# Kernel tuning notes

Hardware: AMD Instinct MI355X
Metric: run time of the kernel (lower is better)

Reference implementation:

```python
import jax, jax.numpy as jnp
import numpy as np

N_NODES = 50000
N_EDGES = 800000
NODE_IN = 10
EDGE_IN = 7
H = 128
N_LAYERS = 6
OUT_DIM = 3


def setup_inputs() -> dict:
    key = jax.random.key(0)
    ks = jax.random.split(key, 32)
    s = 0.05
    inp = {
        "x": jax.random.normal(ks[0], (N_NODES, NODE_IN), jnp.float32),
        "edge_attr": jax.random.normal(ks[1], (N_EDGES, EDGE_IN), jnp.float32),
        "edge_index": jax.random.randint(ks[2], (2, N_EDGES), 0, N_NODES, jnp.int32),
        "bc_disp": jax.random.uniform(ks[3], (N_NODES, 1), jnp.float32),
        "bc_rot": jax.random.uniform(ks[4], (N_NODES, 1), jnp.float32),
        # node encoder: MLP(10, [H], H)
        "ne_w1": jax.random.normal(ks[5], (NODE_IN, H), jnp.float32) * s,
        "ne_b1": jnp.zeros((H,), jnp.float32),
        "ne_w2": jax.random.normal(ks[6], (H, H), jnp.float32) * s,
        "ne_b2": jnp.zeros((H,), jnp.float32),
        # edge encoder: MLP(7, [H], H)
        "ee_w1": jax.random.normal(ks[7], (EDGE_IN, H), jnp.float32) * s,
        "ee_b1": jnp.zeros((H,), jnp.float32),
        "ee_w2": jax.random.normal(ks[8], (H, H), jnp.float32) * s,
        "ee_b2": jnp.zeros((H,), jnp.float32),
        # 6 GraphNetworkLayers: edge model (3H -> H), node model (2H -> H)
        "mp_ew": jax.random.normal(ks[9], (N_LAYERS, 3 * H, H), jnp.float32) * s,
        "mp_eb": jnp.zeros((N_LAYERS, H), jnp.float32),
        "mp_nw": jax.random.normal(ks[10], (N_LAYERS, 2 * H, H), jnp.float32) * s,
        "mp_nb": jnp.zeros((N_LAYERS, H), jnp.float32),
        "d_w1": jax.random.normal(ks[11], (H, H), jnp.float32) * s,
        "d_b1": jnp.zeros((H,), jnp.float32),
        "d_w2": jax.random.normal(ks[12], (H, 64), jnp.float32) * s,
        "d_b2": jnp.zeros((64,), jnp.float32),
        "d_w3": jax.random.normal(ks[13], (64, OUT_DIM), jnp.float32) * (s * 5.0),
        "d_b3": jnp.full((OUT_DIM,), 0.5, jnp.float32),
    }
    return inp


def reference(x, edge_attr, edge_index, bc_disp, bc_rot,
              ne_w1, ne_b1, ne_w2, ne_b2,
              ee_w1, ee_b1, ee_w2, ee_b2,
              mp_ew, mp_eb, mp_nw, mp_nb,
              d_w1, d_b1, d_w2, d_b2, d_w3, d_b3):
    # encode nodes and edges (Linear -> ReLU -> Linear)
    h = jax.nn.relu(x @ ne_w1 + ne_b1) @ ne_w2 + ne_b2            # [N, H]
    e = jax.nn.relu(edge_attr @ ee_w1 + ee_b1) @ ee_w2 + ee_b2    # [E, H]
    src = edge_index[0]
    dst = edge_index[1]
    # 6 residual message-passing layers: gather -> edge MLP -> scatter-add -> node MLP
    for l in range(N_LAYERS):
        msg_in = jnp.concatenate([h[src], h[dst], e], axis=-1)    # [E, 3H]
        msg = jax.nn.relu(msg_in @ mp_ew[l] + mp_eb[l])           # [E, H]
        agg = jax.ops.segment_sum(msg, dst, num_segments=N_NODES)  # [N, H] (aggr='add')
        upd = jax.nn.relu(jnp.concatenate([h, agg], axis=-1) @ mp_nw[l] + mp_nb[l])
        h = h + upd                                               # residual
    # decode: Linear -> ReLU -> Linear -> ReLU -> Linear
    z = jax.nn.relu(h @ d_w1 + d_b1)
    z = jax.nn.relu(z @ d_w2 + d_b2)
    pred = z @ d_w3 + d_b3                                        # [N, 3]
    # hard boundary conditions
    pred = jnp.concatenate([pred[:, 0:2] * (1.0 - bc_disp),
                            pred[:, 2:3] * (1.0 - bc_rot)], axis=-1)
    return pred
```

## Files before the change

kernel.cpp:

```cpp
#include <hip/hip_runtime.h>
#include <hip/hip_bf16.h>

#define NN 50000
#define NE 800000
#define H 128

typedef __hip_bfloat16 bf16;
typedef __attribute__((ext_vector_type(8))) short short8v;
typedef __attribute__((ext_vector_type(4))) float f32x4;

static __device__ __forceinline__ unsigned short f2bf_bits(float x) {
  union { __hip_bfloat16 b; unsigned short u; } cv;
  cv.b = __float2bfloat16(x);
  return cv.u;
}

__global__ __launch_bounds__(256) void fuse_w3_kernel(
    const float* __restrict__ ee_w2, const float* __restrict__ ee_b2,
    const float* __restrict__ mp_ew, const float* __restrict__ mp_eb,
    float* __restrict__ W3p, float* __restrict__ c3)
{
  const int l = blockIdx.x >> 3;
  const int cc = (blockIdx.x & 7) * 16;
  __shared__ float sA[H * H];
  __shared__ float sB[H * 16];
  const float* W3 = mp_ew + (size_t)l * 384 * H + 256 * H;
  for (int i = threadIdx.x; i < H * H; i += 256) sA[i] = ee_w2[i];
  for (int i = threadIdx.x; i < H * 16; i += 256) {
    int k = i >> 4, j = i & 15;
    sB[i] = W3[k * H + cc + j];
  }
  __syncthreads();
  float* out = W3p + (size_t)l * H * H;
  for (int i = threadIdx.x; i < H * 16; i += 256) {
    int r = i >> 4, j = i & 15;
    float acc = 0.f;
    #pragma unroll 8
    for (int k = 0; k < H; ++k) acc += sA[r * H + k] * sB[k * 16 + j];
    out[r * H + cc + j] = acc;
  }
  if (threadIdx.x < 16) {
    int j = threadIdx.x;
    float acc = mp_eb[l * H + cc + j];
    for (int k = 0; k < H; ++k) acc += ee_b2[k] * sB[k * 16 + j];
    c3[l * H + cc + j] = acc;
  }
}

__global__ __launch_bounds__(256) void repack_w_kernel(
    const float* __restrict__ src0, size_t lstride, bf16* __restrict__ dst0, int K)
{
  const int l = blockIdx.x;
  const float* src = src0 + (size_t)l * lstride;
  bf16* dst = dst0 + (size_t)l * K * 128;
  const int nkk = K / 32;
  const int nslots = 8 * nkk * 64;
  for (int idx = threadIdx.x; idx < nslots; idx += 256) {
    int ng = idx / (nkk * 64);
    int rem = idx % (nkk * 64);
    int kk = rem / 64, ln = rem % 64;
    #pragma unroll
    for (int j = 0; j < 8; ++j) {
      int k = kk * 32 + ((ln >> 4) * 8) + j;
      int col = ng * 16 + (ln & 15);
      dst[(size_t)idx * 8 + j] = __float2bfloat16(src[(size_t)k * 128 + col]);
    }
  }
}

__global__ __launch_bounds__(256) void node_encoder_kernel(
    const float* __restrict__ in,
    const float* __restrict__ w1, const float* __restrict__ b1,
    const float* __restrict__ w2, const float* __restrict__ b2,
    float* __restrict__ out, int nrows)
{
  __shared__ float sw1[10 * H];
  __shared__ float sw2[H * H];
  __shared__ float sb1[H];
  __shared__ float sb2[H];
  __shared__ float sin_[8][10];
  __shared__ float st[8][H];

  for (int i = threadIdx.x; i < 10 * H; i += 256) sw1[i] = w1[i];
  for (int i = threadIdx.x; i < H * H; i += 256) sw2[i] = w2[i];
  if (threadIdx.x < H) { sb1[threadIdx.x] = b1[threadIdx.x]; sb2[threadIdx.x] = b2[threadIdx.x]; }
  __syncthreads();

  const int c = threadIdx.x & 127;
  const int hf = threadIdx.x >> 7;

  for (long long r0 = (long long)blockIdx.x * 8; r0 < nrows; r0 += (long long)gridDim.x * 8) {
    if (threadIdx.x < 80) {
      int j = threadIdx.x / 10, k = threadIdx.x % 10;
      long long r = r0 + j;
      sin_[j][k] = (r < nrows) ? in[r * 10 + k] : 0.f;
    }
    __syncthreads();
    #pragma unroll
    for (int t = 0; t < 4; ++t) {
      int idx = threadIdx.x + t * 256;
      int j = idx >> 7, k = idx & 127;
      float acc = sb1[k];
      #pragma unroll
      for (int i = 0; i < 10; ++i) acc += sin_[j][i] * sw1[i * H + k];
      st[j][k] = fmaxf(acc, 0.f);
    }
    __syncthreads();
    float a0 = sb2[c], a1 = a0, a2 = a0, a3 = a0;
    #pragma unroll 4
    for (int k4 = 0; k4 < H; k4 += 4) {
      float w0 = sw2[(k4 + 0) * H + c];
      float w1v = sw2[(k4 + 1) * H + c];
      float w2v = sw2[(k4 + 2) * H + c];
      float w3v = sw2[(k4 + 3) * H + c];
      float4 s0 = *(const float4*)&st[hf * 4 + 0][k4];
      float4 s1 = *(const float4*)&st[hf * 4 + 1][k4];
      float4 s2 = *(const float4*)&st[hf * 4 + 2][k4];
      float4 s3 = *(const float4*)&st[hf * 4 + 3][k4];
      a0 += s0.x * w0 + s0.y * w1v + s0.z * w2v + s0.w * w3v;
      a1 += s1.x * w0 + s1.y * w1v + s1.z * w2v + s1.w * w3v;
      a2 += s2.x * w0 + s2.y * w1v + s2.z * w2v + s2.w * w3v;
      a3 += s3.x * w0 + s3.y * w1v + s3.z * w2v + s3.w * w3v;
    }
    float accs[4] = {a0, a1, a2, a3};
    #pragma unroll
    for (int j = 0; j < 4; ++j) {
      long long r = r0 + hf * 4 + j;
      if (r < nrows) out[r * H + c] = accs[j];
    }
    __syncthreads();
  }
}

__global__ __launch_bounds__(512) void node_AB_kernel(
    const float* __restrict__ h, const float* __restrict__ W1f, const float* __restrict__ W2f,
    bf16* __restrict__ A, bf16* __restrict__ B, float* __restrict__ agg, int nrows)
{
  __shared__ float sw1[H * H];
  __shared__ float sw2[H * H];
  __shared__ float sh[16][H];
  for (int i = threadIdx.x; i < H * H; i += 512) { sw1[i] = W1f[i]; sw2[i] = W2f[i]; }
  __syncthreads();
  const int c = threadIdx.x & 127;
  const int q = threadIdx.x >> 7;
  for (long long r0 = (long long)blockIdx.x * 16; r0 < nrows; r0 += (long long)gridDim.x * 16) {
    #pragma unroll
    for (int t = 0; t < 4; ++t) {
      int idx = threadIdx.x + t * 512;
      int j = idx >> 7, k = idx & 127;
      long long r = r0 + j;
      sh[j][k] = (r < nrows) ? h[r * H + k] : 0.f;
    }
    __syncthreads();
    float aA[4] = {0, 0, 0, 0}, aB[4] = {0, 0, 0, 0};
    #pragma unroll 2
    for (int k4 = 0; k4 < H; k4 += 4) {
      float w10 = sw1[(k4 + 0) * H + c], w11 = sw1[(k4 + 1) * H + c];
      float w12 = sw1[(k4 + 2) * H + c], w13 = sw1[(k4 + 3) * H + c];
      float w20 = sw2[(k4 + 0) * H + c], w21 = sw2[(k4 + 1) * H + c];
      float w22 = sw2[(k4 + 2) * H + c], w23 = sw2[(k4 + 3) * H + c];
      #pragma unroll
      for (int j = 0; j < 4; ++j) {
        float4 s = *(const float4*)&sh[q * 4 + j][k4];
        aA[j] += s.x * w10 + s.y * w11 + s.z * w12 + s.w * w13;
        aB[j] += s.x * w20 + s.y * w21 + s.z * w22 + s.w * w23;
      }
    }
    #pragma unroll
    for (int j = 0; j < 4; ++j) {
      long long r = r0 + q * 4 + j;
      if (r < nrows) {
        A[r * H + c] = __float2bfloat16(aA[j]);
        B[r * H + c] = __float2bfloat16(aB[j]);
        agg[r * H + c] = 0.f;
      }
    }
    __syncthreads();
  }
}

__global__ __launch_bounds__(256) void edge_mfma_scatter(
    const float* __restrict__ ea,
    const int* __restrict__ srcI, const int* __restrict__ dstI,
    const bf16* __restrict__ A, const bf16* __restrict__ B,
    const float* __restrict__ ew1, const float* __restrict__ eb1,
    const bf16* __restrict__ W3b, const float* __restrict__ c3,
    float* __restrict__ agg, int nE)
{
  __shared__ float sew1[7 * H];
  __shared__ float seb1[H];
  __shared__ float sea[32][8];
  __shared__ int   sidx[32];
  __shared__ int   didx[32];
  __shared__ unsigned int shid[32 * 64];

  for (int i = threadIdx.x; i < 7 * H; i += 256) sew1[i] = ew1[i];
  if (threadIdx.x < H) seb1[threadIdx.x] = eb1[threadIdx.x];

  const int t = threadIdx.x;
  const int lane = t & 63;
  const int wid = t >> 6;
  const int colbase = wid * 32;

  short8v bfrag[2][4];
  float c3v[2];
  #pragma unroll
  for (int n = 0; n < 2; ++n) {
    c3v[n] = c3[colbase + n * 16 + (lane & 15)];
    int ng = (colbase >> 4) + n;
    #pragma unroll
    for (int kk = 0; kk < 4; ++kk) {
      const bf16* p = W3b + ((size_t)(ng * 4 + kk) * 64 + lane) * 8;
      bfrag[n][kk] = *(const short8v*)p;
    }
  }
  __syncthreads();

  for (long long e0 = (long long)blockIdx.x * 32; e0 < nE; e0 += (long long)gridDim.x * 32) {
    if (t < 224) sea[t / 7][t % 7] = ea[e0 * 7 + t];
    else         sidx[t - 224] = srcI[e0 + (t - 224)];
    if (t < 32)  didx[t] = dstI[e0 + t];
    __syncthreads();

    {
      const int e = t >> 3;
      float r0 = sea[e][0], r1 = sea[e][1], r2 = sea[e][2], r3 = sea[e][3];
      float r4 = sea[e][4], r5 = sea[e][5], r6 = sea[e][6];
      #pragma unroll
      for (int p = 0; p < 8; ++p) {
        int k2 = (t & 7) + 8 * p;
        int k = k2 * 2;
        float a0 = seb1[k], a1 = seb1[k + 1];
        a0 += r0 * sew1[0 * H + k] + r1 * sew1[1 * H + k] + r2 * sew1[2 * H + k]
            + r3 * sew1[3 * H + k] + r4 * sew1[4 * H + k] + r5 * sew1[5 * H + k]
            + r6 * sew1[6 * H + k];
        a1 += r0 * sew1[0 * H + k + 1] + r1 * sew1[1 * H + k + 1] + r2 * sew1[2 * H + k + 1]
            + r3 * sew1[3 * H + k + 1] + r4 * sew1[4 * H + k + 1] + r5 * sew1[5 * H + k + 1]
            + r6 * sew1[6 * H + k + 1];
        a0 = fmaxf(a0, 0.f); a1 = fmaxf(a1, 0.f);
        unsigned int w = (unsigned int)f2bf_bits(a0) | ((unsigned int)f2bf_bits(a1) << 16);
        int off = (e * 256 + k2 * 4) ^ ((e & 7) << 4);
        shid[off >> 2] = w;
      }
    }
    __syncthreads();

    f32x4 acc[2][2];
    const f32x4 z = {0.f, 0.f, 0.f, 0.f};
    acc[0][0] = z; acc[0][1] = z; acc[1][0] = z; acc[1][1] = z;
    #pragma unroll
    for (int m = 0; m < 2; ++m) {
      #pragma unroll
      for (int kk = 0; kk < 4; ++kk) {
        int row = m * 16 + (lane & 15);
        int off = (row * 256 + kk * 64 + (lane >> 4) * 16) ^ ((row & 7) << 4);
        short8v afrag = *(const short8v*)((const char*)shid + off);
        acc[m][0] = __builtin_amdgcn_mfma_f32_16x16x32_bf16(afrag, bfrag[0][kk], acc[m][0], 0, 0, 0);
        acc[m][1] = __builtin_amdgcn_mfma_f32_16x16x32_bf16(afrag, bfrag[1][kk], acc[m][1], 0, 0, 0);
      }
    }

    #pragma unroll
    for (int m = 0; m < 2; ++m) {
      #pragma unroll
      for (int r = 0; r < 4; ++r) {
        int el = m * 16 + (lane >> 4) * 4 + r;
        int s = sidx[el];
        int d = didx[el];
        #pragma unroll
        for (int n = 0; n < 2; ++n) {
          int col = colbase + n * 16 + (lane & 15);
          float v = acc[m][n][r] + c3v[n]
                  + __bfloat162float(A[(size_t)s * H + col])
                  + __bfloat162float(B[(size_t)d * H + col]);
          atomicAdd(&agg[(size_t)d * H + col], fmaxf(v, 0.f));
        }
      }
    }
    __syncthreads();
  }
}

template<int DO_AB>
__global__ __launch_bounds__(256) void fused_update_kernel(
    float* __restrict__ h, const float* __restrict__ aggin,
    const bf16* __restrict__ Wnb, const float* __restrict__ nb,
    const bf16* __restrict__ W1b, const bf16* __restrict__ W2b,
    bf16* __restrict__ A, bf16* __restrict__ B, float* __restrict__ aggz,
    int nrows)
{
  __shared__ unsigned int sKw[32 * 128];
  unsigned short* shnew = (unsigned short*)sKw;

  const int t = threadIdx.x;
  const int lane = t & 63;
  const int wid = t >> 6;
  const int colbase = wid * 32;

  short8v bU[2][8];
  float nbv[2];
  #pragma unroll
  for (int n = 0; n < 2; ++n) {
    int ng = wid * 2 + n;
    nbv[n] = nb[colbase + n * 16 + (lane & 15)];
    #pragma unroll
    for (int kk = 0; kk < 8; ++kk)
      bU[n][kk] = *(const short8v*)(Wnb + ((size_t)(ng * 8 + kk) * 64 + lane) * 8);
  }

  const int ntiles = (nrows + 31) / 32;
  for (int tile = blockIdx.x; tile < ntiles; tile += gridDim.x) {
    const int r0 = tile * 32;
    #pragma unroll
    for (int i = 0; i < 16; ++i) {
      int w = t + i * 256;
      int row = w >> 7, k2 = w & 127;
      int r = r0 + row;
      float v0 = 0.f, v1 = 0.f;
      if (r < nrows) {
        if (k2 < 64) { float2 p = *(const float2*)&h[(size_t)r * H + 2 * k2]; v0 = p.x; v1 = p.y; }
        else         { float2 p = *(const float2*)&aggin[(size_t)r * H + 2 * k2 - 128]; v0 = p.x; v1 = p.y; }
      }
      unsigned int wrd = (unsigned int)f2bf_bits(v0) | ((unsigned int)f2bf_bits(v1) << 16);
      sKw[((w * 4) ^ ((row & 7) << 4)) >> 2] = wrd;
    }
    __syncthreads();

    f32x4 acc[2][2];
    const f32x4 z = {0.f, 0.f, 0.f, 0.f};
    acc[0][0] = z; acc[0][1] = z; acc[1][0] = z; acc[1][1] = z;
    #pragma unroll
    for (int kk = 0; kk < 8; ++kk) {
      #pragma unroll
      for (int m = 0; m < 2; ++m) {
        int row = m * 16 + (lane & 15);
        int off = (row * 512 + kk * 64 + (lane >> 4) * 16) ^ ((row & 7) << 4);
        short8v afrag = *(const short8v*)((const char*)sKw + off);
        acc[m][0] = __builtin_amdgcn_mfma_f32_16x16x32_bf16(afrag, bU[0][kk], acc[m][0], 0, 0, 0);
        acc[m][1] = __builtin_amdgcn_mfma_f32_16x16x32_bf16(afrag, bU[1][kk], acc[m][1], 0, 0, 0);
      }
    }
    __syncthreads();

    #pragma unroll
    for (int m = 0; m < 2; ++m) {
      #pragma unroll
      for (int r = 0; r < 4; ++r) {
        int row = m * 16 + (lane >> 4) * 4 + r;
        int grow = r0 + row;
        #pragma unroll
        for (int n = 0; n < 2; ++n) {
          int col = colbase + n * 16 + (lane & 15);
          float u = fmaxf(acc[m][n][r] + nbv[n], 0.f);
          float hold = (grow < nrows) ? h[(size_t)grow * H + col] : 0.f;
          float hn = hold + u;
          if (grow < nrows) h[(size_t)grow * H + col] = hn;
          if (DO_AB) {
            int i16 = (row * 128 + col) ^ ((row & 7) << 3);
            shnew[i16] = f2bf_bits(hn);
          }
        }
      }
    }

    if (DO_AB) {
      __syncthreads();
      short8v bA[2][4], bB[2][4];
      #pragma unroll
      for (int n = 0; n < 2; ++n) {
        int ng = wid * 2 + n;
        #pragma unroll
        for (int kk = 0; kk < 4; ++kk) {
          bA[n][kk] = *(const short8v*)(W1b + ((size_t)(ng * 4 + kk) * 64 + lane) * 8);
          bB[n][kk] = *(const short8v*)(W2b + ((size_t)(ng * 4 + kk) * 64 + lane) * 8);
        }
      }
      f32x4 aA[2][2], aB2[2][2];
      aA[0][0] = z; aA[0][1] = z; aA[1][0] = z; aA[1][1] = z;
      aB2[0][0] = z; aB2[0][1] = z; aB2[1][0] = z; aB2[1][1] = z;
      #pragma unroll
      for (int kk = 0; kk < 4; ++kk) {
        #pragma unroll
        for (int m = 0; m < 2; ++m) {
          int row = m * 16 + (lane & 15);
          int off = (row * 256 + kk * 64 + (lane >> 4) * 16) ^ ((row & 7) << 4);
          short8v afrag = *(const short8v*)((const char*)shnew + off);
          aA[m][0] = __builtin_amdgcn_mfma_f32_16x16x32_bf16(afrag, bA[0][kk], aA[m][0], 0, 0, 0);
          aA[m][1] = __builtin_amdgcn_mfma_f32_16x16x32_bf16(afrag, bA[1][kk], aA[m][1], 0, 0, 0);
          aB2[m][0] = __builtin_amdgcn_mfma_f32_16x16x32_bf16(afrag, bB[0][kk], aB2[m][0], 0, 0, 0);
          aB2[m][1] = __builtin_amdgcn_mfma_f32_16x16x32_bf16(afrag, bB[1][kk], aB2[m][1], 0, 0, 0);
        }
      }
      #pragma unroll
      for (int m = 0; m < 2; ++m) {
        #pragma unroll
        for (int r = 0; r < 4; ++r) {
          int row = m * 16 + (lane >> 4) * 4 + r;
          int grow = r0 + row;
          if (grow < nrows) {
            #pragma unroll
            for (int n = 0; n < 2; ++n) {
              int col = colbase + n * 16 + (lane & 15);
              A[(size_t)grow * H + col] = __float2bfloat16(aA[m][n][r]);
              B[(size_t)grow * H + col] = __float2bfloat16(aB2[m][n][r]);
              aggz[(size_t)grow * H + col] = 0.f;
            }
          }
        }
      }
    }
    __syncthreads();
  }
}

__global__ __launch_bounds__(512) void decoder_kernel(
    const float* __restrict__ h,
    const float* __restrict__ w1, const float* __restrict__ b1,
    const float* __restrict__ w2, const float* __restrict__ b2,
    const float* __restrict__ w3, const float* __restrict__ b3,
    const float* __restrict__ bcd, const float* __restrict__ bcr,
    float* __restrict__ out, int nrows)
{
  __shared__ float sw1[H * H];
  __shared__ float sw2[H * 64];
  __shared__ float sw3[64 * 3];
  __shared__ float sb1[H], sb2[64], sb3[3];
  __shared__ float sh[16][H], st1[16][H], st2[16][64];
  for (int i = threadIdx.x; i < H * H; i += 512) sw1[i] = w1[i];
  for (int i = threadIdx.x; i < H * 64; i += 512) sw2[i] = w2[i];
  if (threadIdx.x < 64 * 3) sw3[threadIdx.x] = w3[threadIdx.x];
  if (threadIdx.x < H) sb1[threadIdx.x] = b1[threadIdx.x];
  if (threadIdx.x < 64) sb2[threadIdx.x] = b2[threadIdx.x];
  if (threadIdx.x < 3) sb3[threadIdx.x] = b3[threadIdx.x];
  __syncthreads();
  for (long long r0 = (long long)blockIdx.x * 16; r0 < nrows; r0 += (long long)gridDim.x * 16) {
    #pragma unroll
    for (int t = 0; t < 4; ++t) {
      int idx = threadIdx.x + t * 512;
      int j = idx >> 7, k = idx & 127;
      long long r = r0 + j;
      sh[j][k] = (r < nrows) ? h[r * H + k] : 0.f;
    }
    __syncthreads();
    #pragma unroll
    for (int t = 0; t < 4; ++t) {
      int idx = threadIdx.x + t * 512;
      int j = idx >> 7, k = idx & 127;
      float acc = sb1[k];
      #pragma unroll 8
      for (int i = 0; i < H; ++i) acc += sh[j][i] * sw1[i * H + k];
      st1[j][k] = fmaxf(acc, 0.f);
    }
    __syncthreads();
    #pragma unroll
    for (int t = 0; t < 2; ++t) {
      int idx = threadIdx.x + t * 512;
      int j = idx >> 6, k = idx & 63;
      float acc = sb2[k];
      #pragma unroll 8
      for (int i = 0; i < H; ++i) acc += st1[j][i] * sw2[i * 64 + k];
      st2[j][k] = fmaxf(acc, 0.f);
    }
    __syncthreads();
    if (threadIdx.x < 48) {
      int j = threadIdx.x / 3, o = threadIdx.x % 3;
      float acc = sb3[o];
      #pragma unroll 8
      for (int i = 0; i < 64; ++i) acc += st2[j][i] * sw3[i * 3 + o];
      long long r = r0 + j;
      if (r < nrows) {
        float m = (o < 2) ? (1.f - bcd[r]) : (1.f - bcr[r]);
        out[r * 3 + o] = acc * m;
      }
    }
    __syncthreads();
  }
}

extern "C" void kernel_launch(void* const* d_in, const int* in_sizes, int n_in,
                              void* d_out, int out_size, void* d_ws, size_t ws_size,
                              hipStream_t stream) {
  const float* x     = (const float*)d_in[0];
  const float* ea    = (const float*)d_in[1];
  const int*   eidx  = (const int*)d_in[2];
  const float* bcd   = (const float*)d_in[3];
  const float* bcr   = (const float*)d_in[4];
  const float* ne_w1 = (const float*)d_in[5];
  const float* ne_b1 = (const float*)d_in[6];
  const float* ne_w2 = (const float*)d_in[7];
  const float* ne_b2 = (const float*)d_in[8];
  const float* ee_w1 = (const float*)d_in[9];
  const float* ee_b1 = (const float*)d_in[10];
  const float* ee_w2 = (const float*)d_in[11];
  const float* ee_b2 = (const float*)d_in[12];
  const float* mp_ew = (const float*)d_in[13];
  const float* mp_eb = (const float*)d_in[14];
  const float* mp_nw = (const float*)d_in[15];
  const float* mp_nb = (const float*)d_in[16];
  const float* d_w1  = (const float*)d_in[17];
  const float* d_b1  = (const float*)d_in[18];
  const float* d_w2  = (const float*)d_in[19];
  const float* d_b2  = (const float*)d_in[20];
  const float* d_w3  = (const float*)d_in[21];
  const float* d_b3  = (const float*)d_in[22];

  const int* srcI = eidx;
  const int* dstI = eidx + NE;

  char* wsp = (char*)d_ws;
  float* h    = (float*)wsp; wsp += (size_t)NN * H * 4;
  float* agg  = (float*)wsp; wsp += (size_t)NN * H * 4;
  bf16*  A    = (bf16*)wsp;  wsp += (size_t)NN * H * 2;
  bf16*  B    = (bf16*)wsp;  wsp += (size_t)NN * H * 2;
  bf16*  W3b  = (bf16*)wsp;  wsp += (size_t)6 * H * H * 2;
  bf16*  Wnb  = (bf16*)wsp;  wsp += (size_t)6 * 256 * H * 2;
  bf16*  W1b  = (bf16*)wsp;  wsp += (size_t)6 * H * H * 2;
  bf16*  W2b  = (bf16*)wsp;  wsp += (size_t)6 * H * H * 2;
  float* c3   = (float*)wsp; wsp += (size_t)6 * H * 4;
  float* W3p  = agg;

  fuse_w3_kernel<<<48, 256, 0, stream>>>(ee_w2, ee_b2, mp_ew, mp_eb, W3p, c3);
  repack_w_kernel<<<6, 256, 0, stream>>>(W3p, (size_t)H * H, W3b, 128);
  repack_w_kernel<<<6, 256, 0, stream>>>(mp_nw, (size_t)256 * H, Wnb, 256);
  repack_w_kernel<<<6, 256, 0, stream>>>(mp_ew, (size_t)384 * H, W1b, 128);
  repack_w_kernel<<<6, 256, 0, stream>>>(mp_ew + 128 * H, (size_t)384 * H, W2b, 128);

  node_encoder_kernel<<<2048, 256, 0, stream>>>(x, ne_w1, ne_b1, ne_w2, ne_b2, h, NN);
  node_AB_kernel<<<1024, 512, 0, stream>>>(h, mp_ew, mp_ew + 128 * H, A, B, agg, NN);

  for (int l = 0; l < 6; ++l) {
    edge_mfma_scatter<<<4096, 256, 0, stream>>>(ea, srcI, dstI, A, B, ee_w1, ee_b1,
                                                W3b + (size_t)l * H * H, c3 + l * H, agg, NE);
    if (l < 5) {
      fused_update_kernel<1><<<512, 256, 0, stream>>>(
          h, agg, Wnb + (size_t)l * 256 * H, mp_nb + l * H,
          W1b + (size_t)(l + 1) * H * H, W2b + (size_t)(l + 1) * H * H,
          A, B, agg, NN);
    } else {
      fused_update_kernel<0><<<512, 256, 0, stream>>>(
          h, agg, Wnb + (size_t)l * 256 * H, mp_nb + l * H,
          nullptr, nullptr, nullptr, nullptr, nullptr, NN);
    }
  }

  decoder_kernel<<<1024, 512, 0, stream>>>(h, d_w1, d_b1, d_w2, d_b2, d_w3, d_b3,
                                           bcd, bcr, (float*)d_out, NN);
}
```

Measured before the change: 2.990 ms.

## Sort edges by destination once and pre-reduce messages before atomic scatter

Adds a one-time counting sort (histogram, single-block scan, scatter) that reorders edges by destination node and stores edge attributes as bf16. The edge kernel then walks these sorted arrays, and each lane sums consecutive messages that share a destination in registers before issuing one atomic add per run. The goal is fewer global atomics and better locality for the B-row and agg accesses across the six layers. In exchange it adds four preprocessing kernels, including a slow serial single-block scan over 50k nodes, and it rounds edge attributes to bf16, which slightly changes accuracy.

```diff
diff --git a/kernel.cpp b/kernel.cpp
--- a/kernel.cpp
+++ b/kernel.cpp
@@ -13,6 +13,57 @@
   union { __hip_bfloat16 b; unsigned short u; } cv;
   cv.b = __float2bfloat16(x);
   return cv.u;
+}
+
+__global__ __launch_bounds__(256) void zero_counts_kernel(int* __restrict__ counts) {
+  int i = blockIdx.x * 256 + threadIdx.x;
+  if (i < NN) counts[i] = 0;
+}
+
+__global__ __launch_bounds__(256) void hist_kernel(const int* __restrict__ dstI,
+                                                   int* __restrict__ counts) {
+  int e = blockIdx.x * 256 + threadIdx.x;
+  if (e < NE) atomicAdd(&counts[dstI[e]], 1);
+}
+
+__global__ __launch_bounds__(256) void scan_kernel(const int* __restrict__ counts,
+                                                   int* __restrict__ cursor) {
+  __shared__ int sdata[256];
+  __shared__ int sbase;
+  const int t = threadIdx.x;
+  if (t == 0) sbase = 0;
+  __syncthreads();
+  for (int c0 = 0; c0 < NN; c0 += 256) {
+    int i = c0 + t;
+    int v = (i < NN) ? counts[i] : 0;
+    sdata[t] = v;
+    __syncthreads();
+    #pragma unroll
+    for (int off = 1; off < 256; off <<= 1) {
+      int x = (t >= off) ? sdata[t - off] : 0;
+      __syncthreads();
+      sdata[t] += x;
+      __syncthreads();
+    }
+    if (i < NN) cursor[i] = sbase + sdata[t] - v;
+    __syncthreads();
+    if (t == 255) sbase += sdata[255];
+    __syncthreads();
+  }
+}
+
+__global__ __launch_bounds__(256) void scatter_kernel(
+    const float* __restrict__ ea, const int* __restrict__ srcI, const int* __restrict__ dstI,
+    int* __restrict__ cursor, bf16* __restrict__ eap,
+    int* __restrict__ srcp, int* __restrict__ dstp) {
+  int e = blockIdx.x * 256 + threadIdx.x;
+  if (e >= NE) return;
+  int d = dstI[e];
+  int pos = atomicAdd(&cursor[d], 1);
+  srcp[pos] = srcI[e];
+  dstp[pos] = d;
+  #pragma unroll
+  for (int k = 0; k < 7; ++k) eap[(size_t)pos * 7 + k] = __float2bfloat16(ea[(size_t)e * 7 + k]);
 }
 
 __global__ __launch_bounds__(256) void fuse_w3_kernel(
@@ -180,8 +231,8 @@
 }
 
 __global__ __launch_bounds__(256) void edge_mfma_scatter(
-    const float* __restrict__ ea,
-    const int* __restrict__ srcI, const int* __restrict__ dstI,
+    const bf16* __restrict__ eap,
+    const int* __restrict__ srcp, const int* __restrict__ dstp,
     const bf16* __restrict__ A, const bf16* __restrict__ B,
     const float* __restrict__ ew1, const float* __restrict__ eb1,
     const bf16* __restrict__ W3b, const float* __restrict__ c3,
@@ -217,9 +268,9 @@
   __syncthreads();
 
   for (long long e0 = (long long)blockIdx.x * 32; e0 < nE; e0 += (long long)gridDim.x * 32) {
-    if (t < 224) sea[t / 7][t % 7] = ea[e0 * 7 + t];
-    else         sidx[t - 224] = srcI[e0 + (t - 224)];
-    if (t < 32)  didx[t] = dstI[e0 + t];
+    if (t < 224) sea[t / 7][t % 7] = __bfloat162float(eap[e0 * 7 + t]);
+    else         sidx[t - 224] = srcp[e0 + (t - 224)];
+    if (t < 32)  didx[t] = dstp[e0 + t];
     __syncthreads();
 
     {
@@ -260,22 +311,35 @@
       }
     }
 
+    const int col0 = colbase + (lane & 15);
+    const int col1 = col0 + 16;
     #pragma unroll
     for (int m = 0; m < 2; ++m) {
+      float vs0 = 0.f, vs1 = 0.f;
+      float b0 = 0.f, b1 = 0.f;
+      int dprev = -1;
       #pragma unroll
       for (int r = 0; r < 4; ++r) {
         int el = m * 16 + (lane >> 4) * 4 + r;
         int s = sidx[el];
         int d = didx[el];
-        #pragma unroll
-        for (int n = 0; n < 2; ++n) {
-          int col = colbase + n * 16 + (lane & 15);
-          float v = acc[m][n][r] + c3v[n]
-                  + __bfloat162float(A[(size_t)s * H + col])
-                  + __bfloat162float(B[(size_t)d * H + col]);
-          atomicAdd(&agg[(size_t)d * H + col], fmaxf(v, 0.f));
+        if (d != dprev) {
+          if (dprev >= 0) {
+            atomicAdd(&agg[(size_t)dprev * H + col0], vs0);
+            atomicAdd(&agg[(size_t)dprev * H + col1], vs1);
+          }
+          vs0 = 0.f; vs1 = 0.f;
+          b0 = __bfloat162float(B[(size_t)d * H + col0]);
+          b1 = __bfloat162float(B[(size_t)d * H + col1]);
+          dprev = d;
         }
-      }
+        float a0v = __bfloat162float(A[(size_t)s * H + col0]);
+        float a1v = __bfloat162float(A[(size_t)s * H + col1]);
+        vs0 += fmaxf(acc[m][0][r] + c3v[0] + a0v + b0, 0.f);
+        vs1 += fmaxf(acc[m][1][r] + c3v[1] + a1v + b1, 0.f);
+      }
+      atomicAdd(&agg[(size_t)dprev * H + col0], vs0);
+      atomicAdd(&agg[(size_t)dprev * H + col1], vs1);
     }
     __syncthreads();
   }
@@ -512,12 +576,22 @@
   float* agg  = (float*)wsp; wsp += (size_t)NN * H * 4;
   bf16*  A    = (bf16*)wsp;  wsp += (size_t)NN * H * 2;
   bf16*  B    = (bf16*)wsp;  wsp += (size_t)NN * H * 2;
+  bf16*  eap  = (bf16*)wsp;  wsp += (size_t)NE * 7 * 2;
+  int*   srcp = (int*)wsp;   wsp += (size_t)NE * 4;
+  int*   dstp = (int*)wsp;   wsp += (size_t)NE * 4;
   bf16*  W3b  = (bf16*)wsp;  wsp += (size_t)6 * H * H * 2;
   bf16*  Wnb  = (bf16*)wsp;  wsp += (size_t)6 * 256 * H * 2;
   bf16*  W1b  = (bf16*)wsp;  wsp += (size_t)6 * H * H * 2;
   bf16*  W2b  = (bf16*)wsp;  wsp += (size_t)6 * H * H * 2;
   float* c3   = (float*)wsp; wsp += (size_t)6 * H * 4;
-  float* W3p  = agg;
+  int*   counts = (int*)A;
+  int*   cursor = (int*)A + NN;
+  float* W3p    = agg;
+
+  zero_counts_kernel<<<(NN + 255) / 256, 256, 0, stream>>>(counts);
+  hist_kernel<<<(NE + 255) / 256, 256, 0, stream>>>(dstI, counts);
+  scan_kernel<<<1, 256, 0, stream>>>(counts, cursor);
+  scatter_kernel<<<(NE + 255) / 256, 256, 0, stream>>>(ea, srcI, dstI, cursor, eap, srcp, dstp);
 
   fuse_w3_kernel<<<48, 256, 0, stream>>>(ee_w2, ee_b2, mp_ew, mp_eb, W3p, c3);
   repack_w_kernel<<<6, 256, 0, stream>>>(W3p, (size_t)H * H, W3b, 128);
@@ -529,7 +603,7 @@
   node_AB_kernel<<<1024, 512, 0, stream>>>(h, mp_ew, mp_ew + 128 * H, A, B, agg, NN);
 
   for (int l = 0; l < 6; ++l) {
-    edge_mfma_scatter<<<4096, 256, 0, stream>>>(ea, srcI, dstI, A, B, ee_w1, ee_b1,
+    edge_mfma_scatter<<<4096, 256, 0, stream>>>(eap, srcp, dstp, A, B, ee_w1, ee_b1,
                                                 W3b + (size_t)l * H * H, c3 + l * H, agg, NE);
     if (l < 5) {
       fused_update_kernel<1><<<512, 256, 0, stream>>>(
```

Result: faster. 2.919 ms (-2.4%).
